# Performance work log

Measured on AMD Instinct MI355X. Metric: run time of the kernel, lower is better.

The kernel has to match this reference:

```python
import jax, jax.numpy as jnp
import numpy as np

B, N, QDIM = 2, 4096, 768
H, D = 8, 64  # num_head, head_dim; inner_dim = 512
INNER = H * D


def setup_inputs() -> dict:
    key = jax.random.key(0)
    ks = jax.random.split(key, 6)
    s = lambda fan_in: 1.0 / np.sqrt(fan_in)
    return {
        "x": jax.random.normal(ks[0], (B, N, QDIM), dtype=jnp.float32),
        "Wq": jax.random.normal(ks[1], (QDIM, INNER), dtype=jnp.float32) * s(QDIM),
        "Wk": jax.random.normal(ks[2], (QDIM, INNER), dtype=jnp.float32) * s(QDIM),
        "Wv": jax.random.normal(ks[3], (QDIM, INNER), dtype=jnp.float32) * s(QDIM),
        "Wout": jax.random.normal(ks[4], (INNER, QDIM), dtype=jnp.float32) * s(INNER),
        "b_out": jnp.zeros((QDIM,), dtype=jnp.float32),
    }


def reference(x, Wq, Wk, Wv, Wout, b_out):
    # x: [b, n, q_dim]; self-attention (kv = x), no mask, dropout = 0 (eval).
    scale = D ** -0.5
    # project and split heads: [b, n, h*d] -> [b, h, n, d]
    def heads(t):
        b, n, _ = t.shape
        return t.reshape(b, n, H, D).transpose(0, 2, 1, 3)
    q = heads(x @ Wq)
    k = heads(x @ Wk)
    v = heads(x @ Wv)
    qk = jnp.einsum("bhid,bhjd->bhij", q, k) * scale  # [b, h, n, n] -- O(n^2) matrix
    attn = jax.nn.softmax(qk, axis=-1)
    out = jnp.einsum("bhij,bhjd->bhid", attn, v)  # [b, h, n, d]
    out = out.transpose(0, 2, 1, 3).reshape(x.shape[0], x.shape[1], INNER)
    return out @ Wout + b_out
```

## Files before the change

kernel.cpp:

```cpp
#include <hip/hip_runtime.h>
#include <cstdint>
#include <cstddef>


typedef __attribute__((ext_vector_type(8))) short short8;
typedef __attribute__((ext_vector_type(4))) float f32x4;
typedef __attribute__((ext_vector_type(16))) float f32x16;
typedef __attribute__((ext_vector_type(4))) unsigned int uint4v;

__device__ __forceinline__ unsigned short f2bf(float f) {
  unsigned int u = __float_as_uint(f);
  u = (u + 0x7fffu + ((u >> 16) & 1u)) >> 16;
  return (unsigned short)u;
}

__device__ __forceinline__ float fast_exp2(float x) {
#if __has_builtin(__builtin_amdgcn_exp2f)
  return __builtin_amdgcn_exp2f(x);
#else
  return __expf(x * 0.69314718055994531f);
#endif
}

__device__ __forceinline__ void gld16(const void* g, void* l) {
  __builtin_amdgcn_global_load_lds(
      (__attribute__((address_space(1))) void*)const_cast<void*>(g),
      (__attribute__((address_space(3))) void*)l, 16, 0, 0);
}

__device__ __forceinline__ unsigned int cvtpk_bf16(float lo, float hi) {
  unsigned int r;
  asm("v_cvt_pk_bf16_f32 %0, %1, %2" : "=v"(r) : "v"(lo), "v"(hi));
  return r;
}


__global__ __launch_bounds__(256) void cvt_x_k(const float* __restrict__ x,
                                               unsigned short* __restrict__ xb) {
  const size_t i = ((size_t)blockIdx.x * 256 + threadIdx.x) * 4;
  const float4 v = *(const float4*)(x + i);
  ushort4 u;
  u.x = f2bf(v.x); u.y = f2bf(v.y); u.z = f2bf(v.z); u.w = f2bf(v.w);
  *(ushort4*)(xb + i) = u;
}

__global__ __launch_bounds__(256) void transpose_w_k(
    const float* __restrict__ Wq, const float* __restrict__ Wk,
    const float* __restrict__ Wv, const float* __restrict__ Wout,
    unsigned short* __restrict__ Wt,
    unsigned short* __restrict__ WoT)
{
  __shared__ float t[32][33];
  const int z = blockIdx.z;
  const float* src = (z == 0) ? Wq : (z == 1) ? Wk : (z == 2) ? Wv : Wout;
  const int R = (z < 3) ? 768 : 512, C = (z < 3) ? 512 : 768;
  unsigned short* dst = (z < 3) ? (Wt + (size_t)z * 393216) : WoT;
  const int tx = threadIdx.x & 31, ty = threadIdx.x >> 5;
  const int c0 = blockIdx.x * 32, r0 = blockIdx.y * 32;
  if (c0 >= C || r0 >= R) return;
#pragma unroll
  for (int k = 0; k < 4; ++k)
    t[ty + 8 * k][tx] = src[(size_t)(r0 + ty + 8 * k) * C + c0 + tx];
  __syncthreads();
#pragma unroll
  for (int k = 0; k < 4; ++k)
    dst[(size_t)(c0 + ty + 8 * k) * R + r0 + tx] = f2bf(t[tx][ty + 8 * k]);
}


__global__ __launch_bounds__(256) void gemm_qkv_k(
    const unsigned short* __restrict__ A,
    const unsigned short* __restrict__ Wt,
    unsigned short* __restrict__ qb, unsigned short* __restrict__ kb,
    unsigned short* __restrict__ vtb) {
  __shared__ __align__(16) short Al[4096];
  __shared__ __align__(16) short Bl[4096];
  const int tid = threadIdx.x;
  const int w = tid >> 6, lane = tid & 63, quad = lane >> 4, l15 = lane & 15;
  const int wy = w >> 1, wx = w & 1;
  const int m0 = blockIdx.x * 128, n0 = blockIdx.y * 128;
  const int z = blockIdx.z;
  const unsigned short* Bt = Wt + (size_t)z * (512 * 768);

  f32x4 acc[4][4];
#pragma unroll
  for (int i = 0; i < 4; ++i)
#pragma unroll
    for (int j = 0; j < 4; ++j) acc[i][j] = (f32x4){0.f, 0.f, 0.f, 0.f};

  for (int k0 = 0; k0 < 768; k0 += 32) {
    __syncthreads();
#pragma unroll
    for (int s = 0; s < 2; ++s) {
      const int t = s * 256 + tid;
      gld16(A + (size_t)(m0 + (t >> 2)) * 768 + k0 + (t & 3) * 8,
            Al + s * 2048 + w * 512);
      gld16(Bt + (size_t)(n0 + (t >> 2)) * 768 + k0 + (t & 3) * 8,
            Bl + s * 2048 + w * 512);
    }
    __syncthreads();
    short8 af[4], bf[4];
#pragma unroll
    for (int i = 0; i < 4; ++i) {
      af[i] = *(const short8*)(Al + (wy * 64 + i * 16 + l15) * 32 + quad * 8);
      bf[i] = *(const short8*)(Bl + (wx * 64 + i * 16 + l15) * 32 + quad * 8);
    }
    if (z == 2) {
#pragma unroll
      for (int i = 0; i < 4; ++i)
#pragma unroll
        for (int j = 0; j < 4; ++j)
          acc[i][j] = __builtin_amdgcn_mfma_f32_16x16x32_bf16(af[i], bf[j], acc[i][j], 0, 0, 0);
    } else {
#pragma unroll
      for (int i = 0; i < 4; ++i)
#pragma unroll
        for (int j = 0; j < 4; ++j)
          acc[i][j] = __builtin_amdgcn_mfma_f32_16x16x32_bf16(bf[i], af[j], acc[i][j], 0, 0, 0);
    }
  }

  if (z == 2) {
#pragma unroll
    for (int i = 0; i < 4; ++i) {
#pragma unroll
      for (int j = 0; j < 4; ++j) {
        const int m0r = m0 + wy * 64 + i * 16 + quad * 4;
        const int n = n0 + wx * 64 + j * 16 + l15;
        const int b = m0r >> 12, nseq0 = m0r & 4095;
        const int h = n >> 6, d0 = n & 63;
        const int kti = nseq0 >> 5, kc = (nseq0 >> 4) & 1;
        const int hv = (nseq0 >> 3) & 1, e0 = nseq0 & 7;
        const int dt = (d0 >> 5) & 1, lv = hv * 32 + (d0 & 31);
        ushort4 u;
        u.x = f2bf(acc[i][j][0]); u.y = f2bf(acc[i][j][1]);
        u.z = f2bf(acc[i][j][2]); u.w = f2bf(acc[i][j][3]);
        *(ushort4*)(vtb + (size_t)(b * 8 + h) * 262144 +
                    ((((kti * 2 + dt) * 2 + kc) * 64 + lv) * 8 + e0)) = u;
      }
    }
  } else {
    const float qs = 0.18033688011112042f;
#pragma unroll
    for (int i = 0; i < 4; ++i) {
#pragma unroll
      for (int j = 0; j < 4; ++j) {
        const int n0r = n0 + wx * 64 + i * 16 + quad * 4;
        const int m = m0 + wy * 64 + j * 16 + l15;
        const int b = m >> 12, nseq = m & 4095;
        const int h = n0r >> 6, d0 = n0r & 63;
        ushort4 u;
        if (z == 0) {
          u.x = f2bf(acc[i][j][0] * qs); u.y = f2bf(acc[i][j][1] * qs);
          u.z = f2bf(acc[i][j][2] * qs); u.w = f2bf(acc[i][j][3] * qs);
          *(ushort4*)(qb + (size_t)((b * 8 + h) * 4096 + nseq) * 64 + d0) = u;
        } else {
          const int kti = nseq >> 5, l31k = nseq & 31;
          const int c = (d0 >> 4) & 3, hk = (d0 >> 3) & 1, e0 = d0 & 7;
          u.x = f2bf(acc[i][j][0]); u.y = f2bf(acc[i][j][1]);
          u.z = f2bf(acc[i][j][2]); u.w = f2bf(acc[i][j][3]);
          *(ushort4*)(kb + (size_t)(b * 8 + h) * 262144 +
                      (((kti * 4 + c) * 64 + (hk * 32 + l31k)) * 8 + e0)) = u;
        }
      }
    }
  }
}


__global__ __launch_bounds__(256) void attn_k(
    const unsigned short* __restrict__ qb,
    const unsigned short* __restrict__ kb,
    const unsigned short* __restrict__ vtb,
    unsigned short* __restrict__ ob) {
  __shared__ __align__(16) char smem[34304];
  const int tid = threadIdx.x;
  const int w = tid >> 6, lane = tid & 63;
  const int l31 = lane & 31, hi = lane >> 5;
  const int g = w >> 1, wq = w & 1;

  const int L = blockIdx.x + 32 * blockIdx.y;
  const int bh = ((L & 7) << 1) | ((L >> 3) & 1);
  const int q0 = (L >> 4) << 7;

  const unsigned short* qbase = qb + (size_t)bh * (4096 * 64);
  const unsigned short* kbase = kb + (size_t)bh * 262144 + lane * 8;
  const unsigned short* vbase = vtb + (size_t)bh * 262144 + lane * 8;

  short8 qf[2][4];
#pragma unroll
  for (int qs = 0; qs < 2; ++qs) {
    const int qrow = q0 + wq * 64 + qs * 32 + l31;
#pragma unroll
    for (int c = 0; c < 4; ++c)
      qf[qs][c] = *(const short8*)(qbase + (size_t)qrow * 64 + c * 16 + hi * 8);
  }

  const short one_bf = (short)0x3F80;
  const short8 vones = {one_bf, one_bf, one_bf, one_bf,
                        one_bf, one_bf, one_bf, one_bf};

  f32x16 Oacc[2][2];
#pragma unroll
  for (int qs = 0; qs < 2; ++qs)
#pragma unroll
    for (int dt = 0; dt < 2; ++dt)
#pragma unroll
      for (int r = 0; r < 16; ++r) Oacc[qs][dt][r] = 0.f;
  f32x16 Lacc[2];
#pragma unroll
  for (int qs = 0; qs < 2; ++qs)
#pragma unroll
    for (int r = 0; r < 16; ++r) Lacc[qs][r] = 0.f;

  const int jbase = g * 2048;

  for (int j0 = 0; j0 < 2048; j0 += 64) {
    const int kti0 = (jbase + j0) >> 5;
#pragma unroll
    for (int kt = 0; kt < 2; ++kt) {
      const int kti = kti0 + kt;
      short8 kf[4];
#pragma unroll
      for (int c = 0; c < 4; ++c)
        kf[c] = *(const short8*)(kbase + (size_t)(kti * 4 + c) * 512);
      short8 vf[2][2];
#pragma unroll
      for (int dt = 0; dt < 2; ++dt)
#pragma unroll
        for (int kc = 0; kc < 2; ++kc)
          vf[dt][kc] = *(const short8*)(vbase + (size_t)((kti * 2 + dt) * 2 + kc) * 512);

      uint4v pa[2][2];
#pragma unroll
      for (int qs = 0; qs < 2; ++qs) {
        f32x16 s;
#pragma unroll
        for (int r = 0; r < 16; ++r) s[r] = 0.f;
#pragma unroll
        for (int c = 0; c < 4; ++c)
          s = __builtin_amdgcn_mfma_f32_32x32x16_bf16(kf[c], qf[qs][c], s, 0, 0, 0);

        float e[16];
#pragma unroll
        for (int r = 0; r < 16; ++r) e[r] = fast_exp2(s[r]);

        unsigned int wv[8];
#pragma unroll
        for (int g2 = 0; g2 < 4; ++g2)
#pragma unroll
          for (int p = 0; p < 2; ++p)
            wv[g2 * 2 + p] = cvtpk_bf16(e[4 * g2 + 2 * p], e[4 * g2 + 2 * p + 1]);

        const unsigned int s0 = hi ? wv[0] : wv[2];
        const unsigned int s1 = hi ? wv[1] : wv[3];
        const unsigned int s2 = hi ? wv[4] : wv[6];
        const unsigned int s3 = hi ? wv[5] : wv[7];
        const unsigned int x0 = __shfl_xor(s0, 32, 64);
        const unsigned int x1 = __shfl_xor(s1, 32, 64);
        const unsigned int x2 = __shfl_xor(s2, 32, 64);
        const unsigned int x3 = __shfl_xor(s3, 32, 64);
        pa[qs][0] = (uint4v){hi ? x0 : wv[0], hi ? x1 : wv[1],
                             hi ? wv[2] : x0, hi ? wv[3] : x1};
        pa[qs][1] = (uint4v){hi ? x2 : wv[4], hi ? x3 : wv[5],
                             hi ? wv[6] : x2, hi ? wv[7] : x3};
      }

#pragma unroll
      for (int dt = 0; dt < 2; ++dt)
#pragma unroll
        for (int kc = 0; kc < 2; ++kc)
#pragma unroll
          for (int qs = 0; qs < 2; ++qs)
            Oacc[qs][dt] = __builtin_amdgcn_mfma_f32_32x32x16_bf16(
                __builtin_bit_cast(short8, pa[qs][kc]), vf[dt][kc], Oacc[qs][dt], 0, 0, 0);
#pragma unroll
      for (int kc = 0; kc < 2; ++kc)
#pragma unroll
        for (int qs = 0; qs < 2; ++qs)
          Lacc[qs] = __builtin_amdgcn_mfma_f32_32x32x16_bf16(
              __builtin_bit_cast(short8, pa[qs][kc]), vones, Lacc[qs], 0, 0, 0);
    }
  }

  __syncthreads();
  float* Ox  = (float*)smem;
  float* Lg1 = (float*)(smem + 33792);
  if (g == 1) {
#pragma unroll
    for (int qs = 0; qs < 2; ++qs)
#pragma unroll
      for (int r = 0; r < 16; ++r) {
        const int row = wq * 64 + qs * 32 + (r & 3) + 8 * (r >> 2) + 4 * hi;
        Lg1[row] = Lacc[qs][r];
#pragma unroll
        for (int dt = 0; dt < 2; ++dt)
          Ox[row * 66 + dt * 32 + l31] = Oacc[qs][dt][r];
      }
  }
  __syncthreads();
  if (g == 0) {
    const int b = bh >> 3, h = bh & 7;
#pragma unroll
    for (int qs = 0; qs < 2; ++qs)
#pragma unroll
      for (int r = 0; r < 16; ++r) {
        const int row = wq * 64 + qs * 32 + (r & 3) + 8 * (r >> 2) + 4 * hi;
        const float inv = 1.0f / (Lacc[qs][r] + Lg1[row]);
#pragma unroll
        for (int dt = 0; dt < 2; ++dt)
          ob[(size_t)(b * 4096 + q0 + row) * 512 + h * 64 + dt * 32 + l31] =
              f2bf((Oacc[qs][dt][r] + Ox[row * 66 + dt * 32 + l31]) * inv);
      }
  }
}


__global__ __launch_bounds__(256) void gemm_out_k(
    const unsigned short* __restrict__ A,
    const unsigned short* __restrict__ Bt,
    const float* __restrict__ bias, float* __restrict__ out) {
  __shared__ __align__(16) short Al[4096];
  __shared__ __align__(16) short Bl[2048];
  const int tid = threadIdx.x;
  const int w = tid >> 6, lane = tid & 63, quad = lane >> 4, l15 = lane & 15;
  const int m0 = blockIdx.x * 128, n0 = blockIdx.y * 64;

  f32x4 acc[2][4];
#pragma unroll
  for (int i = 0; i < 2; ++i)
#pragma unroll
    for (int j = 0; j < 4; ++j) acc[i][j] = (f32x4){0.f, 0.f, 0.f, 0.f};

  for (int k0 = 0; k0 < 512; k0 += 32) {
    __syncthreads();
#pragma unroll
    for (int s = 0; s < 2; ++s) {
      const int t = s * 256 + tid;
      gld16(A + (size_t)(m0 + (t >> 2)) * 512 + k0 + (t & 3) * 8,
            Al + s * 2048 + w * 512);
    }
    gld16(Bt + (size_t)(n0 + (tid >> 2)) * 512 + k0 + (tid & 3) * 8,
          Bl + w * 512);
    __syncthreads();
    short8 af[2], bf[4];
#pragma unroll
    for (int i = 0; i < 2; ++i)
      af[i] = *(const short8*)(Al + (w * 32 + i * 16 + l15) * 32 + quad * 8);
#pragma unroll
    for (int j = 0; j < 4; ++j)
      bf[j] = *(const short8*)(Bl + (j * 16 + l15) * 32 + quad * 8);
#pragma unroll
    for (int i = 0; i < 2; ++i)
#pragma unroll
      for (int j = 0; j < 4; ++j)
        acc[i][j] = __builtin_amdgcn_mfma_f32_16x16x32_bf16(bf[j], af[i], acc[i][j], 0, 0, 0);
  }

#pragma unroll
  for (int i = 0; i < 2; ++i) {
#pragma unroll
    for (int j = 0; j < 4; ++j) {
      const int col0 = n0 + j * 16 + quad * 4;
      const int m = m0 + w * 32 + i * 16 + l15;
      const float4 b4 = *(const float4*)(bias + col0);
      float4 o;
      o.x = acc[i][j][0] + b4.x; o.y = acc[i][j][1] + b4.y;
      o.z = acc[i][j][2] + b4.z; o.w = acc[i][j][3] + b4.w;
      *(float4*)(out + (size_t)m * 768 + col0) = o;
    }
  }
}


extern "C" void kernel_launch(void* const* d_in, const int* in_sizes, int n_in,
                              void* d_out, int out_size, void* d_ws, size_t ws_size,
                              hipStream_t stream) {
  const float* x    = (const float*)d_in[0];
  const float* Wq   = (const float*)d_in[1];
  const float* Wk   = (const float*)d_in[2];
  const float* Wv   = (const float*)d_in[3];
  const float* Wout = (const float*)d_in[4];
  const float* bout = (const float*)d_in[5];
  float* out = (float*)d_out;
  char* ws = (char*)d_ws;

  unsigned short* xb  = (unsigned short*)(ws);
  unsigned short* Wt  = (unsigned short*)(ws + 12582912);
  unsigned short* WoT = (unsigned short*)(ws + 14942208);
  unsigned short* qb  = (unsigned short*)(ws + 15728640);
  unsigned short* kb  = (unsigned short*)(ws + 24117248);
  unsigned short* vtb = (unsigned short*)(ws + 32505856);
  unsigned short* ob  = (unsigned short*)(ws + 40894464);

  cvt_x_k<<<6144, 256, 0, stream>>>(x, xb);
  transpose_w_k<<<dim3(24, 24, 4), 256, 0, stream>>>(Wq, Wk, Wv, Wout, Wt, WoT);
  gemm_qkv_k<<<dim3(64, 4, 3), 256, 0, stream>>>(xb, Wt, qb, kb, vtb);
  attn_k<<<dim3(32, 16), 256, 0, stream>>>(qb, kb, vtb, ob);
  gemm_out_k<<<dim3(64, 12), 256, 0, stream>>>(ob, WoT, bout, out);
}
```

Measured before the change: 242.4 us.

## Replace ones-MFMA row sums with VALU sums and permute V layout to drop shuffles

The softmax denominator is now accumulated with scalar adds of the exponentials per lane and combined through one cross-half shuffle and shared memory, instead of extra MFMAs against a ones vector. The V-transposed buffer is written with a permuted key ordering so the exponentiated score registers can be fed directly as the A operand of the PV MFMA, removing the per-tile lane shuffles. s_setprio hints are also placed around the MFMA groups. This removes a quarter of the PV-stage matrix work and the shuffle traffic, at the cost of extra VALU adds and a key-permutation that has to match between producer and consumer.

```diff
diff --git a/kernel.cpp b/kernel.cpp
--- a/kernel.cpp
+++ b/kernel.cpp
@@ -130,7 +130,8 @@
         const int b = m0r >> 12, nseq0 = m0r & 4095;
         const int h = n >> 6, d0 = n & 63;
         const int kti = nseq0 >> 5, kc = (nseq0 >> 4) & 1;
-        const int hv = (nseq0 >> 3) & 1, e0 = nseq0 & 7;
+        const int hv = (nseq0 >> 2) & 1;
+        const int e0 = ((nseq0 >> 3) & 1) * 4;
         const int dt = (d0 >> 5) & 1, lv = hv * 32 + (d0 & 31);
         ushort4 u;
         u.x = f2bf(acc[i][j][0]); u.y = f2bf(acc[i][j][1]);
@@ -173,7 +174,7 @@
     const unsigned short* __restrict__ kb,
     const unsigned short* __restrict__ vtb,
     unsigned short* __restrict__ ob) {
-  __shared__ __align__(16) char smem[34304];
+  __shared__ __align__(16) char smem[34816];
   const int tid = threadIdx.x;
   const int w = tid >> 6, lane = tid & 63;
   const int l31 = lane & 31, hi = lane >> 5;
@@ -196,10 +197,6 @@
       qf[qs][c] = *(const short8*)(qbase + (size_t)qrow * 64 + c * 16 + hi * 8);
   }
 
-  const short one_bf = (short)0x3F80;
-  const short8 vones = {one_bf, one_bf, one_bf, one_bf,
-                        one_bf, one_bf, one_bf, one_bf};
-
   f32x16 Oacc[2][2];
 #pragma unroll
   for (int qs = 0; qs < 2; ++qs)
@@ -207,11 +204,7 @@
     for (int dt = 0; dt < 2; ++dt)
 #pragma unroll
       for (int r = 0; r < 16; ++r) Oacc[qs][dt][r] = 0.f;
-  f32x16 Lacc[2];
-#pragma unroll
-  for (int qs = 0; qs < 2; ++qs)
-#pragma unroll
-    for (int r = 0; r < 16; ++r) Lacc[qs][r] = 0.f;
+  float lsum[2] = {0.f, 0.f};
 
   const int jbase = g * 2048;
 
@@ -237,13 +230,17 @@
         f32x16 s;
 #pragma unroll
         for (int r = 0; r < 16; ++r) s[r] = 0.f;
+        __builtin_amdgcn_s_setprio(1);
 #pragma unroll
         for (int c = 0; c < 4; ++c)
           s = __builtin_amdgcn_mfma_f32_32x32x16_bf16(kf[c], qf[qs][c], s, 0, 0, 0);
+        __builtin_amdgcn_s_setprio(0);
 
         float e[16];
 #pragma unroll
         for (int r = 0; r < 16; ++r) e[r] = fast_exp2(s[r]);
+        lsum[qs] += (((e[0] + e[1]) + (e[2] + e[3])) + ((e[4] + e[5]) + (e[6] + e[7]))) +
+                    (((e[8] + e[9]) + (e[10] + e[11])) + ((e[12] + e[13]) + (e[14] + e[15])));
 
         unsigned int wv[8];
 #pragma unroll
@@ -252,20 +249,11 @@
           for (int p = 0; p < 2; ++p)
             wv[g2 * 2 + p] = cvtpk_bf16(e[4 * g2 + 2 * p], e[4 * g2 + 2 * p + 1]);
 
-        const unsigned int s0 = hi ? wv[0] : wv[2];
-        const unsigned int s1 = hi ? wv[1] : wv[3];
-        const unsigned int s2 = hi ? wv[4] : wv[6];
-        const unsigned int s3 = hi ? wv[5] : wv[7];
-        const unsigned int x0 = __shfl_xor(s0, 32, 64);
-        const unsigned int x1 = __shfl_xor(s1, 32, 64);
-        const unsigned int x2 = __shfl_xor(s2, 32, 64);
-        const unsigned int x3 = __shfl_xor(s3, 32, 64);
-        pa[qs][0] = (uint4v){hi ? x0 : wv[0], hi ? x1 : wv[1],
-                             hi ? wv[2] : x0, hi ? wv[3] : x1};
-        pa[qs][1] = (uint4v){hi ? x2 : wv[4], hi ? x3 : wv[5],
-                             hi ? wv[6] : x2, hi ? wv[7] : x3};
+        pa[qs][0] = (uint4v){wv[0], wv[1], wv[2], wv[3]};
+        pa[qs][1] = (uint4v){wv[4], wv[5], wv[6], wv[7]};
       }
 
+      __builtin_amdgcn_s_setprio(1);
 #pragma unroll
       for (int dt = 0; dt < 2; ++dt)
 #pragma unroll
@@ -274,29 +262,31 @@
           for (int qs = 0; qs < 2; ++qs)
             Oacc[qs][dt] = __builtin_amdgcn_mfma_f32_32x32x16_bf16(
                 __builtin_bit_cast(short8, pa[qs][kc]), vf[dt][kc], Oacc[qs][dt], 0, 0, 0);
-#pragma unroll
-      for (int kc = 0; kc < 2; ++kc)
-#pragma unroll
-        for (int qs = 0; qs < 2; ++qs)
-          Lacc[qs] = __builtin_amdgcn_mfma_f32_32x32x16_bf16(
-              __builtin_bit_cast(short8, pa[qs][kc]), vones, Lacc[qs], 0, 0, 0);
-    }
-  }
+      __builtin_amdgcn_s_setprio(0);
+    }
+  }
+
+  float lt[2];
+#pragma unroll
+  for (int qs = 0; qs < 2; ++qs)
+    lt[qs] = lsum[qs] + __shfl_xor(lsum[qs], 32, 64);
 
   __syncthreads();
-  float* Ox  = (float*)smem;
-  float* Lg1 = (float*)(smem + 33792);
+  float* Ox = (float*)smem;
+  float* Lx = (float*)(smem + 33792);
+#pragma unroll
+  for (int qs = 0; qs < 2; ++qs)
+    Lx[g * 128 + wq * 64 + qs * 32 + l31] = lt[qs];
   if (g == 1) {
 #pragma unroll
     for (int qs = 0; qs < 2; ++qs)
 #pragma unroll
-      for (int r = 0; r < 16; ++r) {
-        const int row = wq * 64 + qs * 32 + (r & 3) + 8 * (r >> 2) + 4 * hi;
-        Lg1[row] = Lacc[qs][r];
-#pragma unroll
-        for (int dt = 0; dt < 2; ++dt)
+      for (int dt = 0; dt < 2; ++dt)
+#pragma unroll
+        for (int r = 0; r < 16; ++r) {
+          const int row = wq * 64 + qs * 32 + (r & 3) + 8 * (r >> 2) + 4 * hi;
           Ox[row * 66 + dt * 32 + l31] = Oacc[qs][dt][r];
-      }
+        }
   }
   __syncthreads();
   if (g == 0) {
@@ -306,7 +296,7 @@
 #pragma unroll
       for (int r = 0; r < 16; ++r) {
         const int row = wq * 64 + qs * 32 + (r & 3) + 8 * (r >> 2) + 4 * hi;
-        const float inv = 1.0f / (Lacc[qs][r] + Lg1[row]);
+        const float inv = 1.0f / (Lx[row] + Lx[128 + row]);
 #pragma unroll
         for (int dt = 0; dt < 2; ++dt)
           ob[(size_t)(b * 4096 + q0 + row) * 512 + h * 64 + dt * 32 + l31] =
```

After: 217.2 us, median of 3. 10.4% less time.
